# Kernel tuning notes

Hardware: AMD Instinct MI355X
Metric: run time of the kernel (lower is better)

The kernel has to match this reference:

```python
import jax, jax.numpy as jnp
import numpy as np

GRAPH_BIAS_SCALE = 0.8
COMMITMENT_COST = 0.01

B, S, L, N = 4, 2048, 512, 8192
D = 2 * L  # codebook feature dim


def setup_inputs() -> dict:
    key = jax.random.key(0)
    ks = jax.random.split(key, 9)
    gw_real = jax.random.normal(ks[0], (B, S, L), dtype=jnp.float32)
    gw_imag = jax.random.normal(ks[1], (B, S, L), dtype=jnp.float32)
    prev_symbol_idx = jax.random.randint(ks[2], (B, S), 0, N)
    codebook = jax.random.uniform(ks[3], (N, D), jnp.float32, -0.5, 0.5)
    adjacency = 0.1 * jax.random.normal(ks[4], (N, N), dtype=jnp.float32)
    sal_w = 0.02 * jax.random.normal(ks[5], (D, 1), dtype=jnp.float32)
    sal_b = jnp.zeros((1,), jnp.float32)
    conf_w = 0.02 * jax.random.normal(ks[6], (D, 1), dtype=jnp.float32)
    conf_b = jnp.zeros((1,), jnp.float32)
    return dict(gw_real=gw_real, gw_imag=gw_imag, prev_symbol_idx=prev_symbol_idx,
                codebook=codebook, adjacency=adjacency,
                sal_w=sal_w, sal_b=sal_b, conf_w=conf_w, conf_b=conf_b)


def reference(gw_real, gw_imag, prev_symbol_idx, codebook, adjacency,
              sal_w, sal_b, conf_w, conf_b):
    sg = jax.lax.stop_gradient
    # z_flat = cat(real, imag): [B, S, D]
    z = jnp.concatenate([gw_real, gw_imag], axis=-1)
    # squared euclidean distances to codebook: [B, S, N]
    d = (jnp.sum(z * z, axis=-1, keepdims=True)
         + jnp.sum(codebook * codebook, axis=-1)
         - 2.0 * jnp.einsum('bsd,nd->bsn', z, codebook))
    # graph prior bias from adjacency rows of previous symbols
    graph_prior = adjacency[prev_symbol_idx]            # [B, S, N]
    d = d - GRAPH_BIAS_SCALE * jax.nn.sigmoid(graph_prior)
    min_indices = jnp.argmin(d, axis=-1)                # [B, S]
    z_q = codebook[min_indices]                         # [B, S, D]
    loss_vq = jnp.mean((z_q - sg(z)) ** 2)
    loss_commit = jnp.mean((sg(z_q) - z) ** 2)
    # straight-through estimator
    z_q_st = z + sg(z_q - z)
    dist_score = -jnp.min(d, axis=-1, keepdims=True)    # [B, S, 1]
    salience = z_q_st @ sal_w + sal_b + 0.1 * dist_score
    confidence = jax.nn.sigmoid(z_q_st @ conf_w + conf_b)
    total_loss = loss_vq + COMMITMENT_COST * loss_commit
    proposal_real = z_q_st[..., :L]
    proposal_imag = z_q_st[..., L:]
    return (proposal_real, proposal_imag, salience, confidence, total_loss, min_indices)
```

## Files before the change

kernel.cpp:

```cpp
#include <hip/hip_runtime.h>
#include <math.h>

#define RDIM 8192
#define DDIM 1024
#define NDIM 8192
#define LDIM 512
#define KT 16

#define OFF_REAL 0
#define OFF_IMAG 4194304
#define OFF_SAL  8388608
#define OFF_CONF 8396800
#define OFF_LOSS 8404992
#define OFF_IDX  8404993

#define MAXCAND 64
#define MARGIN_Q 76
#define QSCALE 64.0f
#define FLT_BIG 3.4e38f

typedef __attribute__((ext_vector_type(8))) short bf16x8;
typedef __attribute__((ext_vector_type(8))) short short8v;
typedef __attribute__((ext_vector_type(4))) float f32x4;

__device__ __forceinline__ unsigned short f2bf(float x) {
  unsigned u = __builtin_bit_cast(unsigned, x);
  unsigned r = (u + 0x7fff + ((u >> 16) & 1)) >> 16;
  return (unsigned short)r;
}

__device__ __forceinline__ void load_lds16(const void* g, void* l) {
  __builtin_amdgcn_global_load_lds((const __attribute__((address_space(1))) void*)g,
                                   (__attribute__((address_space(3))) void*)l, 16, 0, 0);
}

__device__ __forceinline__ short clampq(float s) {
  int qi = __float2int_rn(s * QSCALE);
  qi = qi > 32767 ? 32767 : (qi < -32767 ? -32767 : qi);
  return (short)qi;
}

__global__ __launch_bounds__(256)
void split_norms_kernel(const float* __restrict__ gw_real, const float* __restrict__ gw_imag,
                        const float* __restrict__ codebook,
                        unsigned short* __restrict__ zh, unsigned short* __restrict__ ch,
                        float* __restrict__ znorm, float* __restrict__ cnorm) {
  const int id = blockIdx.x;
  const int t = threadIdx.x;
  float4 v;
  unsigned short* dst;
  if (id < RDIM) {
    v = (t < 128) ? reinterpret_cast<const float4*>(gw_real + (size_t)id * LDIM)[t]
                  : reinterpret_cast<const float4*>(gw_imag + (size_t)id * LDIM)[t - 128];
    dst = zh;
  } else {
    v = reinterpret_cast<const float4*>(codebook + (size_t)(id - RDIM) * DDIM)[t];
    dst = ch;
  }
  const size_t off = (size_t)(id < RDIM ? id : id - RDIM) * DDIM + t * 4;
  *reinterpret_cast<ushort4*>(dst + off) =
      make_ushort4(f2bf(v.x), f2bf(v.y), f2bf(v.z), f2bf(v.w));
  float s = v.x*v.x + v.y*v.y + v.z*v.z + v.w*v.w;
  __shared__ float red[256];
  red[t] = s;
  __syncthreads();
  for (int st = 128; st > 0; st >>= 1) {
    if (t < st) red[t] += red[t + st];
    __syncthreads();
  }
  if (t == 0) {
    if (id < RDIM) znorm[id] = red[0];
    else           cnorm[id - RDIM] = red[0];
  }
}

#define STAGE(basep, kt, ldsbyte) do {                                        \
    load_lds16((basep) + eo1 + (kt) * 64, L + (ldsbyte) + wid * 1024);        \
    load_lds16((basep) + eo2 + (kt) * 64, L + (ldsbyte) + 8192 + wid * 1024); \
  } while (0)

__global__ __launch_bounds__(512)
void dist_mfma_kernel(const unsigned short* __restrict__ zh, const unsigned short* __restrict__ ch,
                      const float* __restrict__ cnorm, short* __restrict__ q) {
  __shared__ unsigned short ldsbuf[65536];
  char* const L = (char*)ldsbuf;

  const int sidx = (int)blockIdx.x;
  const int sw = (sidx & 7) * 128 + (sidx >> 3);
  const int bm = sw >> 5, bn = sw & 31;
  const int row0 = bm * 256, col0 = bn * 256;

  const int tid = threadIdx.x;
  const int wid = tid >> 6, l = tid & 63;
  const int wm = wid >> 2, wn = wid & 3;
  const int lr = l & 15, lg = l >> 4;

  const int p1 = tid, p2 = tid + 512;
  const int r1 = p1 >> 3, c1 = (p1 & 7) ^ (r1 & 7);
  const int r2 = p2 >> 3, c2 = (p2 & 7) ^ (r2 & 7);
  const int eo1 = r1 * DDIM + c1 * 8;
  const int eo2 = r2 * DDIM + c2 * 8;
  const unsigned short* const az0 = zh + (size_t)row0 * DDIM;
  const unsigned short* const az1 = zh + (size_t)(row0 + 128) * DDIM;
  const unsigned short* const ac0 = ch + (size_t)col0 * DDIM;
  const unsigned short* const ac1 = ch + (size_t)(col0 + 128) * DDIM;

  const int fo0 = lr * 128 + ((lg ^ (lr & 7)) << 4);
  const int fo1 = fo0 ^ 64;

  f32x4 acc[4][8];
#pragma unroll
  for (int i = 0; i < 4; ++i)
#pragma unroll
    for (int j = 0; j < 8; ++j)
      acc[i][j] = (f32x4){0.f, 0.f, 0.f, 0.f};

  bf16x8 cfA[2][2], cfB[2][2], zf[4][2];

  STAGE(az0, 0, 0);
  STAGE(az1, 0, 16384);
  STAGE(ac0, 0, 32768);
  STAGE(ac1, 0, 49152);
  STAGE(ac0, 1, 98304);
  STAGE(ac1, 1, 114688);
  asm volatile("s_waitcnt vmcnt(4)" ::: "memory");
  __builtin_amdgcn_sched_barrier(0);
  __builtin_amdgcn_s_barrier();

  for (int t = 0; t < KT; ++t) {
    const int buf = t & 1, nbuf = buf ^ 1;
    const char* const Ab = L + buf * 65536 + wm * 16384;
    const char* const Bb = L + buf * 65536 + 32768 + wn * 8192;

#pragma unroll
    for (int i = 0; i < 2; ++i) {
      cfA[i][0] = *reinterpret_cast<const bf16x8*>(Bb + i * 2048 + fo0);
      cfA[i][1] = *reinterpret_cast<const bf16x8*>(Bb + i * 2048 + fo1);
    }
#pragma unroll
    for (int j = 0; j < 4; ++j) {
      zf[j][0] = *reinterpret_cast<const bf16x8*>(Ab + j * 2048 + fo0);
      zf[j][1] = *reinterpret_cast<const bf16x8*>(Ab + j * 2048 + fo1);
    }
    if (t + 1 < KT) STAGE(az0, t + 1, nbuf * 65536);
    __builtin_amdgcn_sched_barrier(0);
    __builtin_amdgcn_s_barrier();
    __builtin_amdgcn_s_setprio(1);
#pragma unroll
    for (int kh = 0; kh < 2; ++kh)
#pragma unroll
      for (int i = 0; i < 2; ++i)
#pragma unroll
        for (int j = 0; j < 4; ++j)
          acc[i][j] = __builtin_amdgcn_mfma_f32_16x16x32_bf16(cfA[i][kh], zf[j][kh], acc[i][j], 0, 0, 0);
    __builtin_amdgcn_s_setprio(0);
    __builtin_amdgcn_sched_barrier(0);
    __builtin_amdgcn_s_barrier();

#pragma unroll
    for (int i = 0; i < 2; ++i) {
      cfB[i][0] = *reinterpret_cast<const bf16x8*>(Bb + (2 + i) * 2048 + fo0);
      cfB[i][1] = *reinterpret_cast<const bf16x8*>(Bb + (2 + i) * 2048 + fo1);
    }
    if (t + 1 < KT) STAGE(az1, t + 1, nbuf * 65536 + 16384);
    __builtin_amdgcn_sched_barrier(0);
    __builtin_amdgcn_s_barrier();
    __builtin_amdgcn_s_setprio(1);
#pragma unroll
    for (int kh = 0; kh < 2; ++kh)
#pragma unroll
      for (int i = 0; i < 2; ++i)
#pragma unroll
        for (int j = 0; j < 4; ++j)
          acc[2 + i][j] = __builtin_amdgcn_mfma_f32_16x16x32_bf16(cfB[i][kh], zf[j][kh], acc[2 + i][j], 0, 0, 0);
    __builtin_amdgcn_s_setprio(0);
    __builtin_amdgcn_sched_barrier(0);
    __builtin_amdgcn_s_barrier();

#pragma unroll
    for (int j = 0; j < 4; ++j) {
      zf[j][0] = *reinterpret_cast<const bf16x8*>(Ab + (4 + j) * 2048 + fo0);
      zf[j][1] = *reinterpret_cast<const bf16x8*>(Ab + (4 + j) * 2048 + fo1);
    }
    if (t + 2 < KT) STAGE(ac0, t + 2, buf * 65536 + 32768);
    __builtin_amdgcn_sched_barrier(0);
    __builtin_amdgcn_s_barrier();
    __builtin_amdgcn_s_setprio(1);
#pragma unroll
    for (int kh = 0; kh < 2; ++kh)
#pragma unroll
      for (int i = 0; i < 2; ++i)
#pragma unroll
        for (int j = 0; j < 4; ++j)
          acc[2 + i][4 + j] = __builtin_amdgcn_mfma_f32_16x16x32_bf16(cfB[i][kh], zf[j][kh], acc[2 + i][4 + j], 0, 0, 0);
    __builtin_amdgcn_s_setprio(0);
    __builtin_amdgcn_sched_barrier(0);
    __builtin_amdgcn_s_barrier();

    if (t + 2 < KT) STAGE(ac1, t + 2, buf * 65536 + 49152);
    if (t < KT - 2) { asm volatile("s_waitcnt vmcnt(4)" ::: "memory"); }
    else            { asm volatile("s_waitcnt vmcnt(0)" ::: "memory"); }
    __builtin_amdgcn_sched_barrier(0);
    __builtin_amdgcn_s_barrier();
    __builtin_amdgcn_s_setprio(1);
#pragma unroll
    for (int kh = 0; kh < 2; ++kh)
#pragma unroll
      for (int i = 0; i < 2; ++i)
#pragma unroll
        for (int j = 0; j < 4; ++j)
          acc[i][4 + j] = __builtin_amdgcn_mfma_f32_16x16x32_bf16(cfA[i][kh], zf[j][kh], acc[i][4 + j], 0, 0, 0);
    __builtin_amdgcn_s_setprio(0);
    __builtin_amdgcn_sched_barrier(0);
    __builtin_amdgcn_s_barrier();
  }

  const int czero = col0 + wn * 64;
  const int zzero = row0 + wm * 128;
#pragma unroll
  for (int i = 0; i < 4; ++i) {
    const int cc = czero + i * 16 + lg * 4;
    const float4 cn4 = *reinterpret_cast<const float4*>(cnorm + cc);
#pragma unroll
    for (int j = 0; j < 8; ++j) {
      const int zr = zzero + j * 16 + lr;
      const f32x4 a = acc[i][j];
      *reinterpret_cast<short4*>(q + (size_t)zr * NDIM + cc) =
          make_short4(clampq(cn4.x - 2.0f * a[0]), clampq(cn4.y - 2.0f * a[1]),
                      clampq(cn4.z - 2.0f * a[2]), clampq(cn4.w - 2.0f * a[3]));
    }
  }
}

__global__ __launch_bounds__(256)
void collect_kernel(const short* __restrict__ q, const int* __restrict__ prev,
                    const float* __restrict__ adj, const float* __restrict__ znorm,
                    float* __restrict__ out, float* __restrict__ minfinal,
                    int* __restrict__ idxfinal,
                    int* __restrict__ gcount, int* __restrict__ gcand) {
  __shared__ unsigned s_wmin[4];
  __shared__ int s_cnt;
  __shared__ int s_list[MAXCAND];
  const int row = blockIdx.x;
  const int t = threadIdx.x;
  if (t == 0) s_cnt = 0;
  short8v v[4];
  unsigned kmin = 0xffffffffu;
#pragma unroll
  for (int c = 0; c < 4; ++c) {
    v[c] = *reinterpret_cast<const short8v*>(q + (size_t)row * NDIM + (c * 256 + t) * 8);
#pragma unroll
    for (int j = 0; j < 8; ++j) {
      const int col = (c * 256 + t) * 8 + j;
      const unsigned key = (((unsigned)((int)v[c][j] + 32768)) << 13) | (unsigned)col;
      kmin = (key < kmin) ? key : kmin;
    }
  }
  for (int m = 1; m < 64; m <<= 1) {
    const unsigned o = (unsigned)__shfl_xor((int)kmin, m, 64);
    kmin = (o < kmin) ? o : kmin;
  }
  if ((t & 63) == 0) s_wmin[t >> 6] = kmin;
  __syncthreads();
  unsigned gk = s_wmin[0];
  gk = gk < s_wmin[1] ? gk : s_wmin[1];
  gk = gk < s_wmin[2] ? gk : s_wmin[2];
  gk = gk < s_wmin[3] ? gk : s_wmin[3];
  const int qmin = (int)(gk >> 13) - 32768;
  const int winner = (int)(gk & 8191u);
  const int thr = qmin + MARGIN_Q;
#pragma unroll
  for (int c = 0; c < 4; ++c) {
#pragma unroll
    for (int j = 0; j < 8; ++j) {
      if ((int)v[c][j] <= thr) {
        const int pos = atomicAdd(&s_cnt, 1);
        if (pos < MAXCAND) s_list[pos] = (c * 256 + t) * 8 + j;
      }
    }
  }
  __syncthreads();
  const int cnt = (s_cnt < MAXCAND) ? s_cnt : MAXCAND;
  if (t == 0) {
    gcount[row] = (cnt <= 1) ? 1 : cnt;
    out[OFF_IDX + row] = (float)winner;
    idxfinal[row] = winner;
    if (cnt <= 1) {
      const int p = prev[row];
      const float bias = 0.8f / (1.0f + expf(-adj[(size_t)p * NDIM + winner]));
      minfinal[row] = znorm[row] + (float)qmin * (1.0f / QSCALE) - bias;
    } else {
      minfinal[row] = znorm[row] + (float)qmin * (1.0f / QSCALE);
    }
  }
  if (cnt > 1 && t < cnt) gcand[(size_t)row * MAXCAND + t] = s_list[t];
}

__global__ __launch_bounds__(64)
void refine_kernel(const float* __restrict__ gw_real, const float* __restrict__ gw_imag,
                   const float* __restrict__ codebook, const int* __restrict__ prev,
                   const float* __restrict__ adj, const float* __restrict__ znorm,
                   const float* __restrict__ cnorm,
                   const int* __restrict__ gcount, const int* __restrict__ gcand,
                   float* __restrict__ out, float* __restrict__ minfinal,
                   int* __restrict__ idxfinal) {
  const int row = blockIdx.x;
  const int t = threadIdx.x;
  const int K = gcount[row];
  if (K <= 1) return;
  const int base = t * 16;
  const float* zp = (base < LDIM) ? gw_real + (size_t)row * LDIM + base
                                  : gw_imag + (size_t)row * LDIM + (base - LDIM);
  float z[16];
#pragma unroll
  for (int c = 0; c < 4; ++c) {
    const float4 v = reinterpret_cast<const float4*>(zp)[c];
    z[c*4+0] = v.x; z[c*4+1] = v.y; z[c*4+2] = v.z; z[c*4+3] = v.w;
  }
  const float zn = znorm[row];
  const int p = prev[row];
  float bestd = FLT_BIG;
  int besti = 0x7fffffff;
  for (int j = 0; j < K; ++j) {
    const int idx = gcand[(size_t)row * MAXCAND + j];
    const float* cp = codebook + (size_t)idx * DDIM + base;
    float dot = 0.f;
#pragma unroll
    for (int c = 0; c < 4; ++c) {
      const float4 v = reinterpret_cast<const float4*>(cp)[c];
      dot += z[c*4+0]*v.x + z[c*4+1]*v.y + z[c*4+2]*v.z + z[c*4+3]*v.w;
    }
    for (int m = 1; m < 64; m <<= 1) dot += __shfl_xor(dot, m, 64);
    const float d = zn + cnorm[idx] - 2.0f * dot
                  - 0.8f / (1.0f + expf(-adj[(size_t)p * NDIM + idx]));
    if (d < bestd || (d == bestd && idx < besti)) { bestd = d; besti = idx; }
  }
  if (t == 0) {
    out[OFF_IDX + row] = (float)besti;
    minfinal[row] = bestd;
    idxfinal[row] = besti;
  }
}


__global__ __launch_bounds__(256)
void epilogue_kernel(const float* __restrict__ gw_real, const float* __restrict__ gw_imag,
                     const float* __restrict__ codebook,
                     const float* __restrict__ sal_w, const float* __restrict__ sal_b,
                     const float* __restrict__ conf_w, const float* __restrict__ conf_b,
                     const float* __restrict__ minfinal, const int* __restrict__ idxfinal,
                     float* __restrict__ out, float* __restrict__ rowloss) {
  const int row = blockIdx.x;
  const int t = threadIdx.x;
  const int k = t << 2;
  const int idx = idxfinal[row];
  const float4 qv = *reinterpret_cast<const float4*>(codebook + (size_t)idx * DDIM + k);
  float4 z;
  if (k < LDIM) z = *reinterpret_cast<const float4*>(gw_real + (size_t)row * LDIM + k);
  else          z = *reinterpret_cast<const float4*>(gw_imag + (size_t)row * LDIM + (k - LDIM));
  const float dx = qv.x - z.x, dy = qv.y - z.y, dz = qv.z - z.z, dw = qv.w - z.w;
  float4 st;
  st.x = z.x + dx; st.y = z.y + dy; st.z = z.z + dz; st.w = z.w + dw;
  float* dst = (k < LDIM) ? (out + OFF_REAL + (size_t)row * LDIM + k)
                          : (out + OFF_IMAG + (size_t)row * LDIM + (k - LDIM));
  *reinterpret_cast<float4*>(dst) = st;
  const float4 sw = *reinterpret_cast<const float4*>(sal_w + k);
  const float4 cw = *reinterpret_cast<const float4*>(conf_w + k);
  const float sdot = st.x*sw.x + st.y*sw.y + st.z*sw.z + st.w*sw.w;
  const float cdot = st.x*cw.x + st.y*cw.y + st.z*cw.z + st.w*cw.w;
  const float dif = dx*dx + dy*dy + dz*dz + dw*dw;
  __shared__ float r1[256], r2[256], r3[256];
  r1[t] = sdot; r2[t] = cdot; r3[t] = dif;
  __syncthreads();
  for (int s = 128; s > 0; s >>= 1) {
    if (t < s) { r1[t] += r1[t + s]; r2[t] += r2[t + s]; r3[t] += r3[t + s]; }
    __syncthreads();
  }
  if (t == 0) {
    out[OFF_SAL + row]  = r1[0] + sal_b[0] + 0.1f * (-minfinal[row]);
    out[OFF_CONF + row] = 1.0f / (1.0f + expf(-(r2[0] + conf_b[0])));
    rowloss[row] = r3[0];
  }
}

__global__ __launch_bounds__(256)
void loss_kernel(const float* __restrict__ rowloss, float* __restrict__ out) {
  const int t = threadIdx.x;
  float s = 0.f;
  for (int i = t; i < RDIM; i += 256) s += rowloss[i];
  __shared__ float red[256];
  red[t] = s;
  __syncthreads();
  for (int st = 128; st > 0; st >>= 1) {
    if (t < st) red[t] += red[t + st];
    __syncthreads();
  }
  if (t == 0) {
    const float m = red[0] / (float)((size_t)RDIM * DDIM);
    out[OFF_LOSS] = m + 0.01f * m;
  }
}


__global__ __launch_bounds__(256)
void norms_kernel(const float* __restrict__ gw_real, const float* __restrict__ gw_imag,
                  const float* __restrict__ codebook,
                  float* __restrict__ znorm, float* __restrict__ cnorm) {
  const int id = blockIdx.x;
  const int t = threadIdx.x;
  float s;
  if (id < RDIM) {
    const float4* zr = reinterpret_cast<const float4*>(gw_real + (size_t)id * LDIM);
    const float4* zi = reinterpret_cast<const float4*>(gw_imag + (size_t)id * LDIM);
    const float4 v = (t < 128) ? zr[t] : zi[t - 128];
    s = v.x*v.x + v.y*v.y + v.z*v.z + v.w*v.w;
  } else {
    const float4* c = reinterpret_cast<const float4*>(codebook + (size_t)(id - RDIM) * DDIM);
    const float4 v = c[t];
    s = v.x*v.x + v.y*v.y + v.z*v.z + v.w*v.w;
  }
  __shared__ float red[256];
  red[t] = s;
  __syncthreads();
  for (int st = 128; st > 0; st >>= 1) {
    if (t < st) red[t] += red[t + st];
    __syncthreads();
  }
  if (t == 0) {
    if (id < RDIM) znorm[id] = red[0];
    else           cnorm[id - RDIM] = red[0];
  }
}

__global__ __launch_bounds__(256)
void dist_kernel(const float* __restrict__ gw_real, const float* __restrict__ gw_imag,
                 const float* __restrict__ codebook, const int* __restrict__ prev,
                 const float* __restrict__ adj, const float* __restrict__ znorm,
                 const float* __restrict__ cnorm,
                 float* __restrict__ ws_min, int* __restrict__ ws_idx) {
  __shared__ float As[16][64];
  __shared__ float Bs[16][64];
  __shared__ int prevs[64];
  const int bm = blockIdx.x, bn = blockIdx.y;
  const int row0 = bm * 64, col0 = bn * 64;
  const int tid = threadIdx.x;
  const int tx = tid & 15, ty = tid >> 4;
  if (tid < 64) prevs[tid] = prev[row0 + tid];
  const int lm = tid >> 2;
  const int lk = (tid & 3) << 2;
  const int arow = row0 + lm;
  const int brow = col0 + lm;
  float acc[4][4] = {{0.f,0.f,0.f,0.f},{0.f,0.f,0.f,0.f},{0.f,0.f,0.f,0.f},{0.f,0.f,0.f,0.f}};
  for (int kk = 0; kk < DDIM; kk += 16) {
    const int k = kk + lk;
    float4 a, b;
    if (k < LDIM) a = *reinterpret_cast<const float4*>(gw_real + (size_t)arow * LDIM + k);
    else          a = *reinterpret_cast<const float4*>(gw_imag + (size_t)arow * LDIM + (k - LDIM));
    b = *reinterpret_cast<const float4*>(codebook + (size_t)brow * DDIM + k);
    __syncthreads();
    As[lk+0][lm]=a.x; As[lk+1][lm]=a.y; As[lk+2][lm]=a.z; As[lk+3][lm]=a.w;
    Bs[lk+0][lm]=b.x; Bs[lk+1][lm]=b.y; Bs[lk+2][lm]=b.z; Bs[lk+3][lm]=b.w;
    __syncthreads();
#pragma unroll
    for (int k2 = 0; k2 < 16; ++k2) {
      const float4 a4 = *reinterpret_cast<const float4*>(&As[k2][ty << 2]);
      const float4 b4 = *reinterpret_cast<const float4*>(&Bs[k2][tx << 2]);
      const float av[4] = {a4.x, a4.y, a4.z, a4.w};
      const float bv[4] = {b4.x, b4.y, b4.z, b4.w};
#pragma unroll
      for (int i = 0; i < 4; ++i)
#pragma unroll
        for (int j = 0; j < 4; ++j)
          acc[i][j] = fmaf(av[i], bv[j], acc[i][j]);
    }
  }
  const float4 cn4 = *reinterpret_cast<const float4*>(cnorm + col0 + (tx << 2));
  const float cnv[4] = {cn4.x, cn4.y, cn4.z, cn4.w};
#pragma unroll
  for (int i = 0; i < 4; ++i) {
    const int rsub = (ty << 2) + i;
    const int row = row0 + rsub;
    const float zn = znorm[row];
    const int p = prevs[rsub];
    const float4 ad4 = *reinterpret_cast<const float4*>(adj + (size_t)p * NDIM + col0 + (tx << 2));
    const float adv[4] = {ad4.x, ad4.y, ad4.z, ad4.w};
    float bv = FLT_BIG;
    int bi = -1;
#pragma unroll
    for (int j = 0; j < 4; ++j) {
      const float bias = 0.8f * (1.0f / (1.0f + expf(-adv[j])));
      const float dv = (zn + cnv[j]) - 2.0f * acc[i][j] - bias;
      const int col = col0 + (tx << 2) + j;
      if (dv < bv) { bv = dv; bi = col; }
    }
    for (int m = 1; m < 16; m <<= 1) {
      const float ov = __shfl_xor(bv, m, 64);
      const int   oi = __shfl_xor(bi, m, 64);
      if (ov < bv || (ov == bv && oi < bi)) { bv = ov; bi = oi; }
    }
    if (tx == 0) {
      ws_min[(size_t)row * 128 + bn] = bv;
      ws_idx[(size_t)row * 128 + bn] = bi;
    }
  }
}

__global__ __launch_bounds__(128)
void argmin_reduce(const float* __restrict__ ws_min, const int* __restrict__ ws_idx,
                   float* __restrict__ out, float* __restrict__ minfinal,
                   int* __restrict__ idxfinal) {
  const int row = blockIdx.x;
  const int t = threadIdx.x;
  __shared__ float sv[128];
  __shared__ int   si[128];
  sv[t] = ws_min[(size_t)row * 128 + t];
  si[t] = ws_idx[(size_t)row * 128 + t];
  __syncthreads();
  for (int s = 64; s > 0; s >>= 1) {
    if (t < s) {
      const float ov = sv[t + s];
      const int   oi = si[t + s];
      if (ov < sv[t] || (ov == sv[t] && oi < si[t])) { sv[t] = ov; si[t] = oi; }
    }
    __syncthreads();
  }
  if (t == 0) {
    out[OFF_IDX + row] = (float)si[0];
    minfinal[row] = sv[0];
    idxfinal[row] = si[0];
  }
}


extern "C" void kernel_launch(void* const* d_in, const int* in_sizes, int n_in,
                              void* d_out, int out_size, void* d_ws, size_t ws_size,
                              hipStream_t stream) {
  const float* gw_real  = (const float*)d_in[0];
  const float* gw_imag  = (const float*)d_in[1];
  const int*   prev     = (const int*)d_in[2];
  const float* codebook = (const float*)d_in[3];
  const float* adj      = (const float*)d_in[4];
  const float* sal_w    = (const float*)d_in[5];
  const float* sal_b    = (const float*)d_in[6];
  const float* conf_w   = (const float*)d_in[7];
  const float* conf_b   = (const float*)d_in[8];
  float* out = (float*)d_out;
  char* ws = (char*)d_ws;

  const size_t matsz = (size_t)RDIM * DDIM;
  const size_t qsz   = (size_t)RDIM * NDIM;
  size_t need = 2 * matsz * 2
              + qsz * 2
              + (size_t)RDIM * MAXCAND * 4
              + 6 * (size_t)RDIM * 4 + 4096;

  if (ws_size >= need) {
    unsigned short* zh = (unsigned short*)ws;
    unsigned short* chh = zh + matsz;
    short* q = (short*)(chh + matsz);
    int*   gcand  = (int*)(q + qsz);
    int*   gcount = gcand + (size_t)RDIM * MAXCAND;
    float* znorm    = (float*)(gcount + RDIM);
    float* cnorm    = znorm + RDIM;
    float* minfinal = cnorm + NDIM;
    int*   idxfinal = (int*)(minfinal + RDIM);
    float* rowloss  = (float*)(idxfinal + RDIM);

    split_norms_kernel<<<RDIM + NDIM, 256, 0, stream>>>(gw_real, gw_imag, codebook,
                                                        zh, chh, znorm, cnorm);
    dist_mfma_kernel<<<1024, 512, 0, stream>>>(zh, chh, cnorm, q);
    collect_kernel<<<RDIM, 256, 0, stream>>>(q, prev, adj, znorm,
                                             out, minfinal, idxfinal, gcount, gcand);
    refine_kernel<<<RDIM, 64, 0, stream>>>(gw_real, gw_imag, codebook, prev, adj,
                                           znorm, cnorm, gcount, gcand,
                                           out, minfinal, idxfinal);
    epilogue_kernel<<<RDIM, 256, 0, stream>>>(gw_real, gw_imag, codebook, sal_w, sal_b,
                                              conf_w, conf_b, minfinal, idxfinal, out, rowloss);
    loss_kernel<<<1, 256, 0, stream>>>(rowloss, out);
  } else {
    float* ws_min   = (float*)ws;
    int*   ws_idx   = (int*)(ws + (size_t)RDIM * 128 * 4);
    float* znorm    = (float*)(ws + (size_t)RDIM * 128 * 8);
    float* cnorm    = znorm + RDIM;
    float* minfinal = cnorm + NDIM;
    int*   idxfinal = (int*)(minfinal + RDIM);
    float* rowloss  = (float*)(idxfinal + RDIM);

    norms_kernel<<<RDIM + NDIM, 256, 0, stream>>>(gw_real, gw_imag, codebook, znorm, cnorm);
    dist_kernel<<<dim3(RDIM / 64, NDIM / 64), 256, 0, stream>>>(
        gw_real, gw_imag, codebook, prev, adj, znorm, cnorm, ws_min, ws_idx);
    argmin_reduce<<<RDIM, 128, 0, stream>>>(ws_min, ws_idx, out, minfinal, idxfinal);
    epilogue_kernel<<<RDIM, 256, 0, stream>>>(gw_real, gw_imag, codebook, sal_w, sal_b,
                                              conf_w, conf_b, minfinal, idxfinal, out, rowloss);
    loss_kernel<<<1, 256, 0, stream>>>(rowloss, out);
  }
}
```

Before: 230.1 us.

## Fuse argmin candidate selection into GEMM epilogue, drop quantized distance matrix

The distance GEMM epilogue no longer writes the full 8192x8192 int16 quantized distance matrix. It computes a per-block row minimum key, merges it globally with atomicMin, and pushes tile-local candidates within the margin into a per-row global list with atomicAdd. A merged select/refine kernel then filters those candidates against the final global minimum and does the exact refinement. This removes a 128MB write and re-read plus the separate collect kernel. In exchange it adds global atomics, two memsets and a larger candidate buffer, which can overflow when blocks push candidates before they know the global minimum.

```diff
diff --git a/kernel.cpp b/kernel.cpp
--- a/kernel.cpp
+++ b/kernel.cpp
@@ -14,13 +14,12 @@
 #define OFF_LOSS 8404992
 #define OFF_IDX  8404993
 
-#define MAXCAND 64
+#define MAXCAND 128
 #define MARGIN_Q 76
 #define QSCALE 64.0f
 #define FLT_BIG 3.4e38f
 
 typedef __attribute__((ext_vector_type(8))) short bf16x8;
-typedef __attribute__((ext_vector_type(8))) short short8v;
 typedef __attribute__((ext_vector_type(4))) float f32x4;
 
 __device__ __forceinline__ unsigned short f2bf(float x) {
@@ -34,10 +33,10 @@
                                    (__attribute__((address_space(3))) void*)l, 16, 0, 0);
 }
 
-__device__ __forceinline__ short clampq(float s) {
+__device__ __forceinline__ int qbias(float s) {
   int qi = __float2int_rn(s * QSCALE);
   qi = qi > 32767 ? 32767 : (qi < -32767 ? -32767 : qi);
-  return (short)qi;
+  return qi + 32768;
 }
 
 __global__ __launch_bounds__(256)
@@ -81,8 +80,12 @@
 
 __global__ __launch_bounds__(512)
 void dist_mfma_kernel(const unsigned short* __restrict__ zh, const unsigned short* __restrict__ ch,
-                      const float* __restrict__ cnorm, short* __restrict__ q) {
+                      const float* __restrict__ cnorm,
+                      unsigned* __restrict__ gkey, int* __restrict__ gcnt,
+                      unsigned* __restrict__ gcand) {
   __shared__ unsigned short ldsbuf[65536];
+  __shared__ unsigned skey[256][4];
+  __shared__ int sthr[256];
   char* const L = (char*)ldsbuf;
 
   const int sidx = (int)blockIdx.x;
@@ -216,98 +219,101 @@
   }
 
   const int czero = col0 + wn * 64;
-  const int zzero = row0 + wm * 128;
+  float cnv[4][4];
 #pragma unroll
   for (int i = 0; i < 4; ++i) {
-    const int cc = czero + i * 16 + lg * 4;
-    const float4 cn4 = *reinterpret_cast<const float4*>(cnorm + cc);
-#pragma unroll
-    for (int j = 0; j < 8; ++j) {
-      const int zr = zzero + j * 16 + lr;
-      const f32x4 a = acc[i][j];
-      *reinterpret_cast<short4*>(q + (size_t)zr * NDIM + cc) =
-          make_short4(clampq(cn4.x - 2.0f * a[0]), clampq(cn4.y - 2.0f * a[1]),
-                      clampq(cn4.z - 2.0f * a[2]), clampq(cn4.w - 2.0f * a[3]));
-    }
-  }
-}
-
-__global__ __launch_bounds__(256)
-void collect_kernel(const short* __restrict__ q, const int* __restrict__ prev,
-                    const float* __restrict__ adj, const float* __restrict__ znorm,
-                    float* __restrict__ out, float* __restrict__ minfinal,
-                    int* __restrict__ idxfinal,
-                    int* __restrict__ gcount, int* __restrict__ gcand) {
-  __shared__ unsigned s_wmin[4];
-  __shared__ int s_cnt;
-  __shared__ int s_list[MAXCAND];
+    const float4 c4 = *reinterpret_cast<const float4*>(cnorm + czero + i * 16 + lg * 4);
+    cnv[i][0] = c4.x; cnv[i][1] = c4.y; cnv[i][2] = c4.z; cnv[i][3] = c4.w;
+  }
+#pragma unroll
+  for (int j = 0; j < 8; ++j) {
+    unsigned kmin = 0xffffffffu;
+#pragma unroll
+    for (int i = 0; i < 4; ++i)
+#pragma unroll
+      for (int reg = 0; reg < 4; ++reg) {
+        const int qb = qbias(cnv[i][reg] - 2.0f * acc[i][j][reg]);
+        const unsigned key = ((unsigned)qb << 13) | (unsigned)(czero + i * 16 + lg * 4 + reg);
+        kmin = key < kmin ? key : kmin;
+      }
+    {
+      unsigned o = (unsigned)__shfl_xor((int)kmin, 16, 64);
+      kmin = o < kmin ? o : kmin;
+      o = (unsigned)__shfl_xor((int)kmin, 32, 64);
+      kmin = o < kmin ? o : kmin;
+    }
+    if (lg == 0) skey[wm * 128 + j * 16 + lr][wn] = kmin;
+  }
+  __syncthreads();
+  if (tid < 256) {
+    unsigned m = skey[tid][0];
+    m = skey[tid][1] < m ? skey[tid][1] : m;
+    m = skey[tid][2] < m ? skey[tid][2] : m;
+    m = skey[tid][3] < m ? skey[tid][3] : m;
+    atomicMin(&gkey[row0 + tid], m);
+    sthr[tid] = (int)(m >> 13) + MARGIN_Q;
+  }
+  __syncthreads();
+#pragma unroll
+  for (int j = 0; j < 8; ++j) {
+    const int rloc = wm * 128 + j * 16 + lr;
+    const int thr = sthr[rloc];
+    const int zr = row0 + rloc;
+#pragma unroll
+    for (int i = 0; i < 4; ++i)
+#pragma unroll
+      for (int reg = 0; reg < 4; ++reg) {
+        const int qb = qbias(cnv[i][reg] - 2.0f * acc[i][j][reg]);
+        if (qb <= thr) {
+          const int pos = atomicAdd(&gcnt[zr], 1);
+          if (pos < MAXCAND)
+            gcand[(size_t)zr * MAXCAND + pos] =
+                ((unsigned)qb << 13) | (unsigned)(czero + i * 16 + lg * 4 + reg);
+        }
+      }
+  }
+}
+
+__global__ __launch_bounds__(64)
+void select_refine_kernel(const float* __restrict__ gw_real, const float* __restrict__ gw_imag,
+                          const float* __restrict__ codebook, const int* __restrict__ prev,
+                          const float* __restrict__ adj, const float* __restrict__ znorm,
+                          const float* __restrict__ cnorm,
+                          const unsigned* __restrict__ gkey, const int* __restrict__ gcnt,
+                          const unsigned* __restrict__ gcand,
+                          float* __restrict__ out, float* __restrict__ minfinal,
+                          int* __restrict__ idxfinal) {
+  __shared__ int fcol[MAXCAND];
+  __shared__ int fcnt_s;
   const int row = blockIdx.x;
   const int t = threadIdx.x;
-  if (t == 0) s_cnt = 0;
-  short8v v[4];
-  unsigned kmin = 0xffffffffu;
-#pragma unroll
-  for (int c = 0; c < 4; ++c) {
-    v[c] = *reinterpret_cast<const short8v*>(q + (size_t)row * NDIM + (c * 256 + t) * 8);
-#pragma unroll
-    for (int j = 0; j < 8; ++j) {
-      const int col = (c * 256 + t) * 8 + j;
-      const unsigned key = (((unsigned)((int)v[c][j] + 32768)) << 13) | (unsigned)col;
-      kmin = (key < kmin) ? key : kmin;
-    }
-  }
-  for (int m = 1; m < 64; m <<= 1) {
-    const unsigned o = (unsigned)__shfl_xor((int)kmin, m, 64);
-    kmin = (o < kmin) ? o : kmin;
-  }
-  if ((t & 63) == 0) s_wmin[t >> 6] = kmin;
-  __syncthreads();
-  unsigned gk = s_wmin[0];
-  gk = gk < s_wmin[1] ? gk : s_wmin[1];
-  gk = gk < s_wmin[2] ? gk : s_wmin[2];
-  gk = gk < s_wmin[3] ? gk : s_wmin[3];
-  const int qmin = (int)(gk >> 13) - 32768;
+  const unsigned gk = gkey[row];
+  const int qmin_b = (int)(gk >> 13);
   const int winner = (int)(gk & 8191u);
-  const int thr = qmin + MARGIN_Q;
-#pragma unroll
-  for (int c = 0; c < 4; ++c) {
-#pragma unroll
-    for (int j = 0; j < 8; ++j) {
-      if ((int)v[c][j] <= thr) {
-        const int pos = atomicAdd(&s_cnt, 1);
-        if (pos < MAXCAND) s_list[pos] = (c * 256 + t) * 8 + j;
-      }
-    }
-  }
-  __syncthreads();
-  const int cnt = (s_cnt < MAXCAND) ? s_cnt : MAXCAND;
-  if (t == 0) {
-    gcount[row] = (cnt <= 1) ? 1 : cnt;
-    out[OFF_IDX + row] = (float)winner;
-    idxfinal[row] = winner;
-    if (cnt <= 1) {
+  const int thr = qmin_b + MARGIN_Q;
+  int cnt = gcnt[row];
+  cnt = cnt > MAXCAND ? MAXCAND : cnt;
+  if (t == 0) fcnt_s = 0;
+  __syncthreads();
+  for (int b = t; b < cnt; b += 64) {
+    const unsigned e = gcand[(size_t)row * MAXCAND + b];
+    if ((int)(e >> 13) <= thr) {
+      const int p = atomicAdd(&fcnt_s, 1);
+      fcol[p] = (int)(e & 8191u);
+    }
+  }
+  __syncthreads();
+  const int K = fcnt_s;
+  if (K <= 1) {
+    if (t == 0) {
       const int p = prev[row];
       const float bias = 0.8f / (1.0f + expf(-adj[(size_t)p * NDIM + winner]));
-      minfinal[row] = znorm[row] + (float)qmin * (1.0f / QSCALE) - bias;
-    } else {
-      minfinal[row] = znorm[row] + (float)qmin * (1.0f / QSCALE);
-    }
-  }
-  if (cnt > 1 && t < cnt) gcand[(size_t)row * MAXCAND + t] = s_list[t];
-}
-
-__global__ __launch_bounds__(64)
-void refine_kernel(const float* __restrict__ gw_real, const float* __restrict__ gw_imag,
-                   const float* __restrict__ codebook, const int* __restrict__ prev,
-                   const float* __restrict__ adj, const float* __restrict__ znorm,
-                   const float* __restrict__ cnorm,
-                   const int* __restrict__ gcount, const int* __restrict__ gcand,
-                   float* __restrict__ out, float* __restrict__ minfinal,
-                   int* __restrict__ idxfinal) {
-  const int row = blockIdx.x;
-  const int t = threadIdx.x;
-  const int K = gcount[row];
-  if (K <= 1) return;
+      out[OFF_IDX + row] = (float)winner;
+      idxfinal[row] = winner;
+      minfinal[row] = znorm[row] + (float)(qmin_b - 32768) * (1.0f / QSCALE) - bias;
+    }
+    return;
+  }
   const int base = t * 16;
   const float* zp = (base < LDIM) ? gw_real + (size_t)row * LDIM + base
                                   : gw_imag + (size_t)row * LDIM + (base - LDIM);
@@ -322,7 +328,7 @@
   float bestd = FLT_BIG;
   int besti = 0x7fffffff;
   for (int j = 0; j < K; ++j) {
-    const int idx = gcand[(size_t)row * MAXCAND + j];
+    const int idx = fcol[j];
     const float* cp = codebook + (size_t)idx * DDIM + base;
     float dot = 0.f;
 #pragma unroll
@@ -548,32 +554,31 @@
   char* ws = (char*)d_ws;
 
   const size_t matsz = (size_t)RDIM * DDIM;
-  const size_t qsz   = (size_t)RDIM * NDIM;
   size_t need = 2 * matsz * 2
-              + qsz * 2
+              + (size_t)RDIM * 4 * 2
               + (size_t)RDIM * MAXCAND * 4
-              + 6 * (size_t)RDIM * 4 + 4096;
+              + 5 * (size_t)RDIM * 4 + 4096;
 
   if (ws_size >= need) {
     unsigned short* zh = (unsigned short*)ws;
     unsigned short* chh = zh + matsz;
-    short* q = (short*)(chh + matsz);
-    int*   gcand  = (int*)(q + qsz);
-    int*   gcount = gcand + (size_t)RDIM * MAXCAND;
-    float* znorm    = (float*)(gcount + RDIM);
+    unsigned* gkey  = (unsigned*)(chh + matsz);
+    int*      gcnt  = (int*)(gkey + RDIM);
+    unsigned* gcand = (unsigned*)(gcnt + RDIM);
+    float* znorm    = (float*)(gcand + (size_t)RDIM * MAXCAND);
     float* cnorm    = znorm + RDIM;
     float* minfinal = cnorm + NDIM;
     int*   idxfinal = (int*)(minfinal + RDIM);
     float* rowloss  = (float*)(idxfinal + RDIM);
 
+    hipMemsetAsync(gkey, 0xFF, (size_t)RDIM * 4, stream);
+    hipMemsetAsync(gcnt, 0, (size_t)RDIM * 4, stream);
     split_norms_kernel<<<RDIM + NDIM, 256, 0, stream>>>(gw_real, gw_imag, codebook,
                                                         zh, chh, znorm, cnorm);
-    dist_mfma_kernel<<<1024, 512, 0, stream>>>(zh, chh, cnorm, q);
-    collect_kernel<<<RDIM, 256, 0, stream>>>(q, prev, adj, znorm,
-                                             out, minfinal, idxfinal, gcount, gcand);
-    refine_kernel<<<RDIM, 64, 0, stream>>>(gw_real, gw_imag, codebook, prev, adj,
-                                           znorm, cnorm, gcount, gcand,
-                                           out, minfinal, idxfinal);
+    dist_mfma_kernel<<<1024, 512, 0, stream>>>(zh, chh, cnorm, gkey, gcnt, gcand);
+    select_refine_kernel<<<RDIM, 64, 0, stream>>>(gw_real, gw_imag, codebook, prev, adj,
+                                                  znorm, cnorm, gkey, gcnt, gcand,
+                                                  out, minfinal, idxfinal);
     epilogue_kernel<<<RDIM, 256, 0, stream>>>(gw_real, gw_imag, codebook, sal_w, sal_b,
                                               conf_w, conf_b, minfinal, idxfinal, out, rowloss);
     loss_kernel<<<1, 256, 0, stream>>>(rowloss, out);
```

After: 372.6 us. +61.9%, slower.

## Make distance GEMM persistent over four column tiles per workgroup

Applied to the files above, without the earlier changes.

The distance MFMA kernel now launches 256 workgroups instead of 1024. Each workgroup walks four consecutive 256-column codebook tiles in one continuous 64-step pipelined K loop, writing quantized distances and zeroing the accumulators after every 16 steps. This hides per-tile pipeline ramp-up and drain, since prefetch of the next column tile's B data overlaps the current tile's epilogue. It also reduces launch granularity to about one workgroup per CU, which risks load imbalance and less latency hiding. The Z rows are reloaded for each column tile.

```diff
diff --git a/kernel.cpp b/kernel.cpp
--- a/kernel.cpp
+++ b/kernel.cpp
@@ -5,7 +5,7 @@
 #define DDIM 1024
 #define NDIM 8192
 #define LDIM 512
-#define KT 16
+#define NKT 64
 
 #define OFF_REAL 0
 #define OFF_IMAG 4194304
@@ -74,9 +74,9 @@
   }
 }
 
-#define STAGE(basep, kt, ldsbyte) do {                                        \
-    load_lds16((basep) + eo1 + (kt) * 64, L + (ldsbyte) + wid * 1024);        \
-    load_lds16((basep) + eo2 + (kt) * 64, L + (ldsbyte) + 8192 + wid * 1024); \
+#define STAGE(basep, koff, ldsbyte) do {                                        \
+    load_lds16((basep) + eo1 + (koff) * 64, L + (ldsbyte) + wid * 1024);        \
+    load_lds16((basep) + eo2 + (koff) * 64, L + (ldsbyte) + 8192 + wid * 1024); \
   } while (0)
 
 __global__ __launch_bounds__(512)
@@ -86,9 +86,9 @@
   char* const L = (char*)ldsbuf;
 
   const int sidx = (int)blockIdx.x;
-  const int sw = (sidx & 7) * 128 + (sidx >> 3);
-  const int bm = sw >> 5, bn = sw & 31;
-  const int row0 = bm * 256, col0 = bn * 256;
+  const int sw = (sidx & 7) * 32 + (sidx >> 3);
+  const int bm = sw >> 3, bg = sw & 7;
+  const int row0 = bm * 256;
 
   const int tid = threadIdx.x;
   const int wid = tid >> 6, l = tid & 63;
@@ -102,8 +102,6 @@
   const int eo2 = r2 * DDIM + c2 * 8;
   const unsigned short* const az0 = zh + (size_t)row0 * DDIM;
   const unsigned short* const az1 = zh + (size_t)(row0 + 128) * DDIM;
-  const unsigned short* const ac0 = ch + (size_t)col0 * DDIM;
-  const unsigned short* const ac1 = ch + (size_t)(col0 + 128) * DDIM;
 
   const int fo0 = lr * 128 + ((lg ^ (lr & 7)) << 4);
   const int fo1 = fo0 ^ 64;
@@ -117,20 +115,26 @@
 
   bf16x8 cfA[2][2], cfB[2][2], zf[4][2];
 
-  STAGE(az0, 0, 0);
-  STAGE(az1, 0, 16384);
-  STAGE(ac0, 0, 32768);
-  STAGE(ac1, 0, 49152);
-  STAGE(ac0, 1, 98304);
-  STAGE(ac1, 1, 114688);
+  {
+    const unsigned short* const b0 = ch + (size_t)(bg * 4 * 256) * DDIM;
+    STAGE(az0, 0, 0);
+    STAGE(az1, 0, 16384);
+    STAGE(b0, 0, 32768);
+    STAGE(b0 + (size_t)128 * DDIM, 0, 49152);
+    STAGE(b0, 1, 98304);
+    STAGE(b0 + (size_t)128 * DDIM, 1, 114688);
+  }
   asm volatile("s_waitcnt vmcnt(4)" ::: "memory");
   __builtin_amdgcn_sched_barrier(0);
   __builtin_amdgcn_s_barrier();
 
-  for (int t = 0; t < KT; ++t) {
+  for (int t = 0; t < NKT; ++t) {
     const int buf = t & 1, nbuf = buf ^ 1;
     const char* const Ab = L + buf * 65536 + wm * 16384;
     const char* const Bb = L + buf * 65536 + 32768 + wn * 8192;
+    const int kA = (t + 1) & 15;
+    const int bt = t + 2;
+    const unsigned short* const bc = ch + (size_t)((bg * 4 + (bt >> 4)) * 256) * DDIM;
 
 #pragma unroll
     for (int i = 0; i < 2; ++i) {
@@ -142,7 +146,7 @@
       zf[j][0] = *reinterpret_cast<const bf16x8*>(Ab + j * 2048 + fo0);
       zf[j][1] = *reinterpret_cast<const bf16x8*>(Ab + j * 2048 + fo1);
     }
-    if (t + 1 < KT) STAGE(az0, t + 1, nbuf * 65536);
+    if (t + 1 < NKT) STAGE(az0, kA, nbuf * 65536);
     __builtin_amdgcn_sched_barrier(0);
     __builtin_amdgcn_s_barrier();
     __builtin_amdgcn_s_setprio(1);
@@ -162,7 +166,7 @@
       cfB[i][0] = *reinterpret_cast<const bf16x8*>(Bb + (2 + i) * 2048 + fo0);
       cfB[i][1] = *reinterpret_cast<const bf16x8*>(Bb + (2 + i) * 2048 + fo1);
     }
-    if (t + 1 < KT) STAGE(az1, t + 1, nbuf * 65536 + 16384);
+    if (t + 1 < NKT) STAGE(az1, kA, nbuf * 65536 + 16384);
     __builtin_amdgcn_sched_barrier(0);
     __builtin_amdgcn_s_barrier();
     __builtin_amdgcn_s_setprio(1);
@@ -182,7 +186,7 @@
       zf[j][0] = *reinterpret_cast<const bf16x8*>(Ab + (4 + j) * 2048 + fo0);
       zf[j][1] = *reinterpret_cast<const bf16x8*>(Ab + (4 + j) * 2048 + fo1);
     }
-    if (t + 2 < KT) STAGE(ac0, t + 2, buf * 65536 + 32768);
+    if (bt < NKT) STAGE(bc, bt & 15, buf * 65536 + 32768);
     __builtin_amdgcn_sched_barrier(0);
     __builtin_amdgcn_s_barrier();
     __builtin_amdgcn_s_setprio(1);
@@ -197,9 +201,9 @@
     __builtin_amdgcn_sched_barrier(0);
     __builtin_amdgcn_s_barrier();
 
-    if (t + 2 < KT) STAGE(ac1, t + 2, buf * 65536 + 49152);
-    if (t < KT - 2) { asm volatile("s_waitcnt vmcnt(4)" ::: "memory"); }
-    else            { asm volatile("s_waitcnt vmcnt(0)" ::: "memory"); }
+    if (bt < NKT) STAGE(bc + (size_t)128 * DDIM, bt & 15, buf * 65536 + 49152);
+    if (t < NKT - 2) { asm volatile("s_waitcnt vmcnt(4)" ::: "memory"); }
+    else             { asm volatile("s_waitcnt vmcnt(0)" ::: "memory"); }
     __builtin_amdgcn_sched_barrier(0);
     __builtin_amdgcn_s_barrier();
     __builtin_amdgcn_s_setprio(1);
@@ -213,21 +217,24 @@
     __builtin_amdgcn_s_setprio(0);
     __builtin_amdgcn_sched_barrier(0);
     __builtin_amdgcn_s_barrier();
-  }
-
-  const int czero = col0 + wn * 64;
-  const int zzero = row0 + wm * 128;
-#pragma unroll
-  for (int i = 0; i < 4; ++i) {
-    const int cc = czero + i * 16 + lg * 4;
-    const float4 cn4 = *reinterpret_cast<const float4*>(cnorm + cc);
-#pragma unroll
-    for (int j = 0; j < 8; ++j) {
-      const int zr = zzero + j * 16 + lr;
-      const f32x4 a = acc[i][j];
-      *reinterpret_cast<short4*>(q + (size_t)zr * NDIM + cc) =
-          make_short4(clampq(cn4.x - 2.0f * a[0]), clampq(cn4.y - 2.0f * a[1]),
-                      clampq(cn4.z - 2.0f * a[2]), clampq(cn4.w - 2.0f * a[3]));
+
+    if ((t & 15) == 15) {
+      const int czero = (bg * 4 + (t >> 4)) * 256 + wn * 64;
+      const int zzero = row0 + wm * 128;
+#pragma unroll
+      for (int i = 0; i < 4; ++i) {
+        const int cc = czero + i * 16 + lg * 4;
+        const float4 cn4 = *reinterpret_cast<const float4*>(cnorm + cc);
+#pragma unroll
+        for (int j = 0; j < 8; ++j) {
+          const int zr = zzero + j * 16 + lr;
+          const f32x4 a = acc[i][j];
+          *reinterpret_cast<short4*>(q + (size_t)zr * NDIM + cc) =
+              make_short4(clampq(cn4.x - 2.0f * a[0]), clampq(cn4.y - 2.0f * a[1]),
+                          clampq(cn4.z - 2.0f * a[2]), clampq(cn4.w - 2.0f * a[3]));
+          acc[i][j] = (f32x4){0.f, 0.f, 0.f, 0.f};
+        }
+      }
     }
   }
 }
@@ -568,7 +575,7 @@
 
     split_norms_kernel<<<RDIM + NDIM, 256, 0, stream>>>(gw_real, gw_imag, codebook,
                                                         zh, chh, znorm, cnorm);
-    dist_mfma_kernel<<<1024, 512, 0, stream>>>(zh, chh, cnorm, q);
+    dist_mfma_kernel<<<256, 512, 0, stream>>>(zh, chh, cnorm, q);
     collect_kernel<<<RDIM, 256, 0, stream>>>(q, prev, adj, znorm,
                                              out, minfinal, idxfinal, gcount, gcand);
     refine_kernel<<<RDIM, 64, 0, stream>>>(gw_real, gw_imag, codebook, prev, adj,
```

Measured after the change: 227.5 us. No clear change (-1.1%).

## Fuse collect and refine kernels, use wave shuffles for norm and epilogue reductions

Applied to the files above, without the earlier changes.

Merges candidate collection and exact refinement into one kernel. The candidate list now stays in LDS, and the four waves split the candidates between them before a cross-wave argmin, so the gcand/gcount global round trip and one launch disappear. The split/norm kernel now handles one row per wave with 16 elements per lane and a shuffle reduction. The epilogue swaps its LDS tree reductions for wave shuffles. These changes cut launch overhead, barriers and LDS traffic, at the cost of more per-lane register work.

```diff
diff --git a/kernel.cpp b/kernel.cpp
--- a/kernel.cpp
+++ b/kernel.cpp
@@ -45,33 +45,38 @@
                         const float* __restrict__ codebook,
                         unsigned short* __restrict__ zh, unsigned short* __restrict__ ch,
                         float* __restrict__ znorm, float* __restrict__ cnorm) {
-  const int id = blockIdx.x;
-  const int t = threadIdx.x;
-  float4 v;
+  const int w = threadIdx.x >> 6, l = threadIdx.x & 63;
+  const int id = blockIdx.x * 4 + w;
+  const float* src;
   unsigned short* dst;
+  float* nrm;
+  int row;
   if (id < RDIM) {
-    v = (t < 128) ? reinterpret_cast<const float4*>(gw_real + (size_t)id * LDIM)[t]
-                  : reinterpret_cast<const float4*>(gw_imag + (size_t)id * LDIM)[t - 128];
-    dst = zh;
+    row = id; dst = zh; nrm = znorm;
+    src = (l < 32) ? gw_real + (size_t)row * LDIM + l * 16
+                   : gw_imag + (size_t)row * LDIM + (l - 32) * 16;
   } else {
-    v = reinterpret_cast<const float4*>(codebook + (size_t)(id - RDIM) * DDIM)[t];
-    dst = ch;
-  }
-  const size_t off = (size_t)(id < RDIM ? id : id - RDIM) * DDIM + t * 4;
-  *reinterpret_cast<ushort4*>(dst + off) =
-      make_ushort4(f2bf(v.x), f2bf(v.y), f2bf(v.z), f2bf(v.w));
-  float s = v.x*v.x + v.y*v.y + v.z*v.z + v.w*v.w;
-  __shared__ float red[256];
-  red[t] = s;
-  __syncthreads();
-  for (int st = 128; st > 0; st >>= 1) {
-    if (t < st) red[t] += red[t + st];
-    __syncthreads();
-  }
-  if (t == 0) {
-    if (id < RDIM) znorm[id] = red[0];
-    else           cnorm[id - RDIM] = red[0];
-  }
+    row = id - RDIM; dst = ch; nrm = cnorm;
+    src = codebook + (size_t)row * DDIM + l * 16;
+  }
+  float f[16];
+#pragma unroll
+  for (int i = 0; i < 4; ++i) {
+    const float4 v = reinterpret_cast<const float4*>(src)[i];
+    f[i*4+0] = v.x; f[i*4+1] = v.y; f[i*4+2] = v.z; f[i*4+3] = v.w;
+  }
+  short8v h0, h1;
+  float s = 0.f;
+#pragma unroll
+  for (int i = 0; i < 8; ++i) { h0[i] = (short)f2bf(f[i]);     s += f[i] * f[i]; }
+#pragma unroll
+  for (int i = 0; i < 8; ++i) { h1[i] = (short)f2bf(f[8 + i]); s += f[8+i] * f[8+i]; }
+  unsigned short* dp = dst + (size_t)row * DDIM + l * 16;
+  *reinterpret_cast<short8v*>(dp)     = h0;
+  *reinterpret_cast<short8v*>(dp + 8) = h1;
+#pragma unroll
+  for (int m = 1; m < 64; m <<= 1) s += __shfl_xor(s, m, 64);
+  if (l == 0) nrm[row] = s;
 }
 
 #define STAGE(basep, kt, ldsbyte) do {                                        \
@@ -233,14 +238,18 @@
 }
 
 __global__ __launch_bounds__(256)
-void collect_kernel(const short* __restrict__ q, const int* __restrict__ prev,
-                    const float* __restrict__ adj, const float* __restrict__ znorm,
-                    float* __restrict__ out, float* __restrict__ minfinal,
-                    int* __restrict__ idxfinal,
-                    int* __restrict__ gcount, int* __restrict__ gcand) {
+void collect_refine_kernel(const short* __restrict__ q, const int* __restrict__ prev,
+                           const float* __restrict__ adj,
+                           const float* __restrict__ gw_real, const float* __restrict__ gw_imag,
+                           const float* __restrict__ codebook,
+                           const float* __restrict__ znorm, const float* __restrict__ cnorm,
+                           float* __restrict__ out, float* __restrict__ minfinal,
+                           int* __restrict__ idxfinal) {
   __shared__ unsigned s_wmin[4];
   __shared__ int s_cnt;
   __shared__ int s_list[MAXCAND];
+  __shared__ float s_bv[4];
+  __shared__ int   s_bi[4];
   const int row = blockIdx.x;
   const int t = threadIdx.x;
   if (t == 0) s_cnt = 0;
@@ -281,64 +290,56 @@
   }
   __syncthreads();
   const int cnt = (s_cnt < MAXCAND) ? s_cnt : MAXCAND;
-  if (t == 0) {
-    gcount[row] = (cnt <= 1) ? 1 : cnt;
-    out[OFF_IDX + row] = (float)winner;
-    idxfinal[row] = winner;
-    if (cnt <= 1) {
+  if (cnt <= 1) {
+    if (t == 0) {
       const int p = prev[row];
       const float bias = 0.8f / (1.0f + expf(-adj[(size_t)p * NDIM + winner]));
+      out[OFF_IDX + row] = (float)winner;
+      idxfinal[row] = winner;
       minfinal[row] = znorm[row] + (float)qmin * (1.0f / QSCALE) - bias;
-    } else {
-      minfinal[row] = znorm[row] + (float)qmin * (1.0f / QSCALE);
-    }
-  }
-  if (cnt > 1 && t < cnt) gcand[(size_t)row * MAXCAND + t] = s_list[t];
-}
-
-__global__ __launch_bounds__(64)
-void refine_kernel(const float* __restrict__ gw_real, const float* __restrict__ gw_imag,
-                   const float* __restrict__ codebook, const int* __restrict__ prev,
-                   const float* __restrict__ adj, const float* __restrict__ znorm,
-                   const float* __restrict__ cnorm,
-                   const int* __restrict__ gcount, const int* __restrict__ gcand,
-                   float* __restrict__ out, float* __restrict__ minfinal,
-                   int* __restrict__ idxfinal) {
-  const int row = blockIdx.x;
-  const int t = threadIdx.x;
-  const int K = gcount[row];
-  if (K <= 1) return;
-  const int base = t * 16;
+    }
+    return;
+  }
+  const int w = t >> 6, l = t & 63;
+  const int base = l * 16;
   const float* zp = (base < LDIM) ? gw_real + (size_t)row * LDIM + base
                                   : gw_imag + (size_t)row * LDIM + (base - LDIM);
   float z[16];
 #pragma unroll
   for (int c = 0; c < 4; ++c) {
-    const float4 v = reinterpret_cast<const float4*>(zp)[c];
-    z[c*4+0] = v.x; z[c*4+1] = v.y; z[c*4+2] = v.z; z[c*4+3] = v.w;
+    const float4 zv = reinterpret_cast<const float4*>(zp)[c];
+    z[c*4+0] = zv.x; z[c*4+1] = zv.y; z[c*4+2] = zv.z; z[c*4+3] = zv.w;
   }
   const float zn = znorm[row];
   const int p = prev[row];
   float bestd = FLT_BIG;
   int besti = 0x7fffffff;
-  for (int j = 0; j < K; ++j) {
-    const int idx = gcand[(size_t)row * MAXCAND + j];
+  for (int j = w; j < cnt; j += 4) {
+    const int idx = s_list[j];
     const float* cp = codebook + (size_t)idx * DDIM + base;
     float dot = 0.f;
 #pragma unroll
     for (int c = 0; c < 4; ++c) {
-      const float4 v = reinterpret_cast<const float4*>(cp)[c];
-      dot += z[c*4+0]*v.x + z[c*4+1]*v.y + z[c*4+2]*v.z + z[c*4+3]*v.w;
+      const float4 cv = reinterpret_cast<const float4*>(cp)[c];
+      dot += z[c*4+0]*cv.x + z[c*4+1]*cv.y + z[c*4+2]*cv.z + z[c*4+3]*cv.w;
     }
     for (int m = 1; m < 64; m <<= 1) dot += __shfl_xor(dot, m, 64);
     const float d = zn + cnorm[idx] - 2.0f * dot
                   - 0.8f / (1.0f + expf(-adj[(size_t)p * NDIM + idx]));
     if (d < bestd || (d == bestd && idx < besti)) { bestd = d; besti = idx; }
   }
+  if (l == 0) { s_bv[w] = bestd; s_bi[w] = besti; }
+  __syncthreads();
   if (t == 0) {
-    out[OFF_IDX + row] = (float)besti;
-    minfinal[row] = bestd;
-    idxfinal[row] = besti;
+    float bv = s_bv[0]; int bi = s_bi[0];
+#pragma unroll
+    for (int w2 = 1; w2 < 4; ++w2) {
+      const float ov = s_bv[w2]; const int oi = s_bi[w2];
+      if (ov < bv || (ov == bv && oi < bi)) { bv = ov; bi = oi; }
+    }
+    out[OFF_IDX + row] = (float)bi;
+    minfinal[row] = bv;
+    idxfinal[row] = bi;
   }
 }
 
@@ -350,8 +351,10 @@
                      const float* __restrict__ conf_w, const float* __restrict__ conf_b,
                      const float* __restrict__ minfinal, const int* __restrict__ idxfinal,
                      float* __restrict__ out, float* __restrict__ rowloss) {
+  __shared__ float s1[4], s2[4], s3[4];
   const int row = blockIdx.x;
   const int t = threadIdx.x;
+  const int w = t >> 6, l = t & 63;
   const int k = t << 2;
   const int idx = idxfinal[row];
   const float4 qv = *reinterpret_cast<const float4*>(codebook + (size_t)idx * DDIM + k);
@@ -366,20 +369,24 @@
   *reinterpret_cast<float4*>(dst) = st;
   const float4 sw = *reinterpret_cast<const float4*>(sal_w + k);
   const float4 cw = *reinterpret_cast<const float4*>(conf_w + k);
-  const float sdot = st.x*sw.x + st.y*sw.y + st.z*sw.z + st.w*sw.w;
-  const float cdot = st.x*cw.x + st.y*cw.y + st.z*cw.z + st.w*cw.w;
-  const float dif = dx*dx + dy*dy + dz*dz + dw*dw;
-  __shared__ float r1[256], r2[256], r3[256];
-  r1[t] = sdot; r2[t] = cdot; r3[t] = dif;
-  __syncthreads();
-  for (int s = 128; s > 0; s >>= 1) {
-    if (t < s) { r1[t] += r1[t + s]; r2[t] += r2[t + s]; r3[t] += r3[t + s]; }
-    __syncthreads();
-  }
+  float r1 = st.x*sw.x + st.y*sw.y + st.z*sw.z + st.w*sw.w;
+  float r2 = st.x*cw.x + st.y*cw.y + st.z*cw.z + st.w*cw.w;
+  float r3 = dx*dx + dy*dy + dz*dz + dw*dw;
+#pragma unroll
+  for (int m = 1; m < 64; m <<= 1) {
+    r1 += __shfl_xor(r1, m, 64);
+    r2 += __shfl_xor(r2, m, 64);
+    r3 += __shfl_xor(r3, m, 64);
+  }
+  if (l == 0) { s1[w] = r1; s2[w] = r2; s3[w] = r3; }
+  __syncthreads();
   if (t == 0) {
-    out[OFF_SAL + row]  = r1[0] + sal_b[0] + 0.1f * (-minfinal[row]);
-    out[OFF_CONF + row] = 1.0f / (1.0f + expf(-(r2[0] + conf_b[0])));
-    rowloss[row] = r3[0];
+    const float t1 = s1[0] + s1[1] + s1[2] + s1[3];
+    const float t2 = s2[0] + s2[1] + s2[2] + s2[3];
+    const float t3 = s3[0] + s3[1] + s3[2] + s3[3];
+    out[OFF_SAL + row]  = t1 + sal_b[0] + 0.1f * (-minfinal[row]);
+    out[OFF_CONF + row] = 1.0f / (1.0f + expf(-(t2 + conf_b[0])));
+    rowloss[row] = t3;
   }
 }
 
@@ -551,29 +558,23 @@
   const size_t qsz   = (size_t)RDIM * NDIM;
   size_t need = 2 * matsz * 2
               + qsz * 2
-              + (size_t)RDIM * MAXCAND * 4
-              + 6 * (size_t)RDIM * 4 + 4096;
+              + 5 * (size_t)RDIM * 4 + 4096;
 
   if (ws_size >= need) {
     unsigned short* zh = (unsigned short*)ws;
     unsigned short* chh = zh + matsz;
     short* q = (short*)(chh + matsz);
-    int*   gcand  = (int*)(q + qsz);
-    int*   gcount = gcand + (size_t)RDIM * MAXCAND;
-    float* znorm    = (float*)(gcount + RDIM);
+    float* znorm    = (float*)(q + qsz);
     float* cnorm    = znorm + RDIM;
     float* minfinal = cnorm + NDIM;
     int*   idxfinal = (int*)(minfinal + RDIM);
     float* rowloss  = (float*)(idxfinal + RDIM);
 
-    split_norms_kernel<<<RDIM + NDIM, 256, 0, stream>>>(gw_real, gw_imag, codebook,
-                                                        zh, chh, znorm, cnorm);
+    split_norms_kernel<<<(RDIM + NDIM) / 4, 256, 0, stream>>>(gw_real, gw_imag, codebook,
+                                                              zh, chh, znorm, cnorm);
     dist_mfma_kernel<<<1024, 512, 0, stream>>>(zh, chh, cnorm, q);
-    collect_kernel<<<RDIM, 256, 0, stream>>>(q, prev, adj, znorm,
-                                             out, minfinal, idxfinal, gcount, gcand);
-    refine_kernel<<<RDIM, 64, 0, stream>>>(gw_real, gw_imag, codebook, prev, adj,
-                                           znorm, cnorm, gcount, gcand,
-                                           out, minfinal, idxfinal);
+    collect_refine_kernel<<<RDIM, 256, 0, stream>>>(q, prev, adj, gw_real, gw_imag, codebook,
+                                                    znorm, cnorm, out, minfinal, idxfinal);
     epilogue_kernel<<<RDIM, 256, 0, stream>>>(gw_real, gw_imag, codebook, sal_w, sal_b,
                                               conf_w, conf_b, minfinal, idxfinal, out, rowloss);
     loss_kernel<<<1, 256, 0, stream>>>(rowloss, out);
```

New measurement: 223.5 us. 2.8% less time.
